# Performance work log

Measured on AMD Instinct MI355X. Metric: run time of the kernel, lower is better.

The kernel has to match this reference:

```python
import jax, jax.numpy as jnp
import numpy as np
import math

B, N, DMODEL, H = 8, 1024, 256, 8
HEAD_DIM = DMODEL // H


def setup_inputs() -> dict:
    key = jax.random.key(0)
    ks = jax.random.split(key, 8)
    x = jax.random.normal(ks[0], (B, N, DMODEL), dtype=jnp.float32)
    # symmetric-ish nonnegative pairwise distances
    adj = jax.random.uniform(ks[1], (B, N, N), dtype=jnp.float32) * 10.0
    mask = jax.random.uniform(ks[2], (B, N)) < 0.9  # bool, mostly valid nodes
    W_qkv = jax.random.normal(ks[3], (DMODEL, 3 * DMODEL), dtype=jnp.float32) / math.sqrt(DMODEL)
    b_qkv = jax.random.normal(ks[4], (3 * DMODEL,), dtype=jnp.float32) * 0.01
    shifts = jnp.arange(1.0, H + 1.0, dtype=jnp.float32)  # initial_shifts
    widths = jnp.ones((H,), dtype=jnp.float32)            # initial_widths
    # self_loop_W = 1/head_dim + U(0,1), non-trainable
    self_loop_w = 1.0 / HEAD_DIM + jax.random.uniform(ks[5], (H,), dtype=jnp.float32)
    return {"x": x, "adj": adj, "mask": mask, "W_qkv": W_qkv, "b_qkv": b_qkv,
            "shifts": shifts, "widths": widths, "self_loop_w": self_loop_w}


def reference(x, adj, mask, W_qkv, b_qkv, shifts, widths, self_loop_w):
    b, n, _ = x.shape
    h = shifts.shape[0]
    d = W_qkv.shape[1] // (3 * h)
    qkv = (x @ W_qkv + b_qkv).reshape(b, n, 3, h, d)
    qkv = jnp.transpose(qkv, (2, 0, 3, 1, 4))  # [3, B, H, N, D]
    Q, K, V = qkv[0], qkv[1], qkv[2]
    scores = jnp.einsum('bhnd,bhmd->bhnm', Q, K) / jnp.sqrt(jnp.float32(d))
    # Gaussian moire focus on adjacency distances, per head
    sh = shifts.reshape(1, h, 1, 1)
    w = jnp.maximum(widths, 0.5).reshape(1, h, 1, 1)
    moire = jnp.exp(-((adj[:, None, :, :] - sh) ** 2) / w)
    adjusted = scores + jnp.log(jnp.maximum(moire, 1e-6))
    eye = jnp.eye(n, dtype=adjusted.dtype)  # [N, N]
    adjusted = adjusted + eye * self_loop_w.reshape(1, h, 1, 1)
    mask2d = (mask[:, :, None] & mask[:, None, :])[:, None, :, :]  # [B,1,N,N]
    adjusted = jnp.where(mask2d, adjusted, jnp.float32(-1000000.0))
    attn = jax.nn.softmax(adjusted, axis=-1)
    out = jnp.einsum('bhnm,bhmd->bhnd', attn, V)
    return jnp.transpose(out, (0, 2, 1, 3)).reshape(b, n, h * d)
```

## Files before the change

kernel.cpp:

```cpp
#include <hip/hip_runtime.h>

#define BB 8
#define NN 1024
#define DM 256
#define HH 8
#define HD 32
#define TC 768

typedef __bf16 bf16x8 __attribute__((ext_vector_type(8)));
typedef float  f32x4  __attribute__((ext_vector_type(4)));

__global__ __launch_bounds__(256, 4) void qkv_gemm(
    const float* __restrict__ x, const float* __restrict__ W,
    const float* __restrict__ bias, __bf16* __restrict__ Qb,
    __bf16* __restrict__ Kb, __bf16* __restrict__ Vt)
{
  __shared__ __align__(16) __bf16 As[128][40];
  __shared__ __align__(16) __bf16 Bs[64][40];
  const int tid  = threadIdx.x;
  const int w    = tid >> 6, lane = tid & 63;
  const int n16  = lane & 15, quad = lane >> 4;
  const int m0   = blockIdx.y * 128, c0 = blockIdx.x * 64;

  const int arow = tid >> 1, ahalf = tid & 1;
  const int bc   = tid & 63, bkh = tid >> 6;

  f32x4 acc[2][4] = {};
  const f32x4 zero = {0.f, 0.f, 0.f, 0.f};
  (void)zero;

  for (int k0 = 0; k0 < DM; k0 += 32) {
    {
      const float* xa = &x[(size_t)(m0 + arow) * DM + k0 + ahalf * 16];
      float4 f0 = *(const float4*)&xa[0];
      float4 f1 = *(const float4*)&xa[4];
      float4 f2 = *(const float4*)&xa[8];
      float4 f3 = *(const float4*)&xa[12];
      bf16x8 a0, a1;
      a0[0]=(__bf16)f0.x; a0[1]=(__bf16)f0.y; a0[2]=(__bf16)f0.z; a0[3]=(__bf16)f0.w;
      a0[4]=(__bf16)f1.x; a0[5]=(__bf16)f1.y; a0[6]=(__bf16)f1.z; a0[7]=(__bf16)f1.w;
      a1[0]=(__bf16)f2.x; a1[1]=(__bf16)f2.y; a1[2]=(__bf16)f2.z; a1[3]=(__bf16)f2.w;
      a1[4]=(__bf16)f3.x; a1[5]=(__bf16)f3.y; a1[6]=(__bf16)f3.z; a1[7]=(__bf16)f3.w;
      *(bf16x8*)&As[arow][ahalf*16]     = a0;
      *(bf16x8*)&As[arow][ahalf*16 + 8] = a1;
    }
    {
      bf16x8 bv;
      #pragma unroll
      for (int j = 0; j < 8; ++j)
        bv[j] = (__bf16)W[(size_t)(k0 + bkh*8 + j) * TC + c0 + bc];
      *(bf16x8*)&Bs[bc][bkh*8] = bv;
    }
    __syncthreads();
    bf16x8 af0 = *(const bf16x8*)&As[w*32 + n16][quad*8];
    bf16x8 af1 = *(const bf16x8*)&As[w*32 + 16 + n16][quad*8];
    #pragma unroll
    for (int cb = 0; cb < 4; ++cb) {
      bf16x8 bf = *(const bf16x8*)&Bs[cb*16 + n16][quad*8];
      acc[0][cb] = __builtin_amdgcn_mfma_f32_16x16x32_bf16(af0, bf, acc[0][cb], 0, 0, 0);
      acc[1][cb] = __builtin_amdgcn_mfma_f32_16x16x32_bf16(af1, bf, acc[1][cb], 0, 0, 0);
    }
    __syncthreads();
  }

  #pragma unroll
  for (int cb = 0; cb < 4; ++cb) {
    const int c = c0 + cb*16 + n16;
    const float bv = bias[c];
    const int s = c >> 8, h = (c >> 5) & 7, dd = c & 31;
    #pragma unroll
    for (int mb = 0; mb < 2; ++mb) {
      #pragma unroll
      for (int r = 0; r < 4; ++r) {
        const int m = m0 + w*32 + mb*16 + quad*4 + r;
        const int bb = m >> 10, n = m & 1023;
        const __bf16 v = (__bf16)(acc[mb][cb][r] + bv);
        if (s == 2)
          Vt[((size_t)((bb*HH + h)*HD + dd))*NN + n] = v;
        else
          ((s == 0) ? Qb : Kb)[((size_t)((bb*HH + h)*NN + n))*HD + dd] = v;
      }
    }
  }
}

__global__ __launch_bounds__(256, 4) void attn_kernel(
    const __bf16* __restrict__ Q, const __bf16* __restrict__ K,
    const __bf16* __restrict__ Vt, const float* __restrict__ adj,
    const int* __restrict__ mask, const float* __restrict__ shifts,
    const float* __restrict__ widths, const float* __restrict__ slw,
    float* __restrict__ out)
{
  __shared__ __align__(16) __bf16 Qs[64][40];
  __shared__ __align__(16) __bf16 Ks[2][64][40];
  __shared__ __align__(16) __bf16 Vts[2][32][72];
  __shared__ __align__(16) __bf16 Ps[64][72];

  const int tid  = threadIdx.x;
  const int w    = tid >> 6, lane = tid & 63;
  const int n16  = lane & 15, quad = lane >> 4;
  const int bh   = blockIdx.x >> 4, qt = blockIdx.x & 15;
  const int b    = bh >> 3, h = bh & 7;
  const int q0   = qt * 64;

  const float L2E   = 1.4426950408889634f;
  const float sh    = shifts[h];
  const float ninvw = -L2E / fmaxf(widths[h], 0.5f);
  const float slv   = slw[h] * L2E;
  const float scl   = 0.17677669529663687f * L2E;
  const float LGEPS = -19.931568569324174f;
  const float MASKV = -28.0f;

  const int srow = tid >> 2, sseg = tid & 3;
  const int vd   = tid >> 3, vsg  = tid & 7;

  {
    const __bf16* Qg = Q + (size_t)(bh*NN + q0)*HD;
    *(bf16x8*)&Qs[srow][sseg*8] = *(const bf16x8*)&Qg[srow*HD + sseg*8];
  }
  const __bf16* Kg = K + (size_t)bh*NN*HD;
  const __bf16* Vg = Vt + (size_t)bh*HD*NN;
  {
    bf16x8 k0v = *(const bf16x8*)&Kg[srow*HD + sseg*8];
    bf16x8 v0v = *(const bf16x8*)&Vg[(size_t)vd*NN + vsg*8];
    *(bf16x8*)&Ks[0][srow][sseg*8] = k0v;
    *(bf16x8*)&Vts[0][vd][vsg*8]   = v0v;
  }
  int mq[4];
  #pragma unroll
  for (int r = 0; r < 4; ++r) mq[r] = mask[b*NN + q0 + w*16 + quad*4 + r];
  __syncthreads();

  const bf16x8 qf = *(const bf16x8*)&Qs[w*16 + n16][quad*8];
  const f32x4 zero = {0.f, 0.f, 0.f, 0.f};
  float l_r[4] = {0.f, 0.f, 0.f, 0.f};
  f32x4 o0 = zero, o1 = zero;

  const float* adjRow = adj + ((size_t)(b*NN + q0 + w*16 + quad*4))*NN;
  const int*   mrow   = mask + b*NN;

  #pragma unroll 2
  for (int jt = 0; jt < 16; ++jt) {
    const int cur = jt & 1;
    const int j0  = jt * 64;

    bf16x8 kn, vn;
    if (jt < 15) {
      kn = *(const bf16x8*)&Kg[(j0 + 64 + srow)*HD + sseg*8];
      vn = *(const bf16x8*)&Vg[(size_t)vd*NN + j0 + 64 + vsg*8];
    }

    int mj[4];
    #pragma unroll
    for (int cb = 0; cb < 4; ++cb) mj[cb] = mrow[j0 + cb*16 + n16];
    float av[4][4];
    #pragma unroll
    for (int r = 0; r < 4; ++r)
      #pragma unroll
      for (int cb = 0; cb < 4; ++cb)
        av[r][cb] = adjRow[(size_t)r*NN + j0 + cb*16 + n16];

    f32x4 s[4];
    #pragma unroll
    for (int cb = 0; cb < 4; ++cb) {
      bf16x8 kf = *(const bf16x8*)&Ks[cur][cb*16 + n16][quad*8];
      s[cb] = __builtin_amdgcn_mfma_f32_16x16x32_bf16(qf, kf, zero, 0, 0, 0);
    }

    #pragma unroll
    for (int r = 0; r < 4; ++r) {
      const int qg = q0 + w*16 + quad*4 + r;
      #pragma unroll
      for (int cb = 0; cb < 4; ++cb) {
        float d   = av[r][cb] - sh;
        float mo  = fmaxf(d*d*ninvw, LGEPS);
        float val = fmaf(s[cb][r], scl, mo);
        if (j0 + cb*16 + n16 == qg) val += slv;
        bool ok = (mq[r] != 0) && (mj[cb] != 0);
        val = ok ? val : MASKV;
        float p = exp2f(val);
        l_r[r] += p;
        Ps[w*16 + quad*4 + r][cb*16 + n16] = (__bf16)p;
      }
    }

    bf16x8 a0  = *(const bf16x8*)&Ps[w*16 + n16][quad*8];
    bf16x8 a1  = *(const bf16x8*)&Ps[w*16 + n16][32 + quad*8];
    bf16x8 b00 = *(const bf16x8*)&Vts[cur][n16][quad*8];
    bf16x8 b01 = *(const bf16x8*)&Vts[cur][n16][32 + quad*8];
    bf16x8 b10 = *(const bf16x8*)&Vts[cur][16 + n16][quad*8];
    bf16x8 b11 = *(const bf16x8*)&Vts[cur][16 + n16][32 + quad*8];
    o0 = __builtin_amdgcn_mfma_f32_16x16x32_bf16(a0, b00, o0, 0, 0, 0);
    o0 = __builtin_amdgcn_mfma_f32_16x16x32_bf16(a1, b01, o0, 0, 0, 0);
    o1 = __builtin_amdgcn_mfma_f32_16x16x32_bf16(a0, b10, o1, 0, 0, 0);
    o1 = __builtin_amdgcn_mfma_f32_16x16x32_bf16(a1, b11, o1, 0, 0, 0);

    if (jt < 15) {
      *(bf16x8*)&Ks[1 - cur][srow][sseg*8] = kn;
      *(bf16x8*)&Vts[1 - cur][vd][vsg*8]   = vn;
    }
    __syncthreads();
  }

  #pragma unroll
  for (int r = 0; r < 4; ++r) {
    float l = l_r[r];
    l += __shfl_xor(l, 1); l += __shfl_xor(l, 2);
    l += __shfl_xor(l, 4); l += __shfl_xor(l, 8);
    const float invl = 1.0f / l;
    const int n = q0 + w*16 + quad*4 + r;
    float* og = out + ((size_t)(b*NN + n))*DM + h*HD;
    og[n16]      = o0[r] * invl;
    og[16 + n16] = o1[r] * invl;
  }
}

extern "C" void kernel_launch(void* const* d_in, const int* in_sizes, int n_in,
                              void* d_out, int out_size, void* d_ws, size_t ws_size,
                              hipStream_t stream) {
  const float* x      = (const float*)d_in[0];
  const float* adj    = (const float*)d_in[1];
  const int*   mask   = (const int*)d_in[2];
  const float* W      = (const float*)d_in[3];
  const float* bias   = (const float*)d_in[4];
  const float* shifts = (const float*)d_in[5];
  const float* widths = (const float*)d_in[6];
  const float* slwp   = (const float*)d_in[7];
  float* out = (float*)d_out;

  __bf16* Qb = (__bf16*)d_ws;
  __bf16* Kb = Qb + (size_t)BB*HH*NN*HD;
  __bf16* Vt = Kb + (size_t)BB*HH*NN*HD;

  qkv_gemm<<<dim3(TC/64, (BB*NN)/128), 256, 0, stream>>>(x, W, bias, Qb, Kb, Vt);
  attn_kernel<<<dim3(BB*HH*(NN/64)), 256, 0, stream>>>(Qb, Kb, Vt, adj, mask,
                                                       shifts, widths, slwp, out);
}
```

Measured before the change: 163.5 us.

## Split attention over key halves with combine kernel, stage QKV epilogue through LDS

The attention kernel is templated to process half of the key range per block (grid y=2). It writes unnormalized partial outputs and row sums to workspace, and a new combine kernel adds the two halves and normalizes. This doubles block count to raise occupancy and parallelism, at the cost of an extra launch and additional fp32 traffic. The QKV GEMM epilogue now stages results through shared memory so Q/K/V^T stores are vectorized and coalesced. Other changes: Qs and Ps share LDS, the diagonal check is restricted to the diagonal tile, and exp2f is replaced with the hardware builtin.

Result: faster. 151.8 us (-7.2%).

```diff
diff --git a/kernel.cpp b/kernel.cpp
--- a/kernel.cpp
+++ b/kernel.cpp
@@ -8,6 +8,7 @@
 #define TC 768
 
 typedef __bf16 bf16x8 __attribute__((ext_vector_type(8)));
+typedef __bf16 bf16x4 __attribute__((ext_vector_type(4)));
 typedef float  f32x4  __attribute__((ext_vector_type(4)));
 
 __global__ __launch_bounds__(256, 4) void qkv_gemm(
@@ -15,19 +16,20 @@
     const float* __restrict__ bias, __bf16* __restrict__ Qb,
     __bf16* __restrict__ Kb, __bf16* __restrict__ Vt)
 {
-  __shared__ __align__(16) __bf16 As[128][40];
-  __shared__ __align__(16) __bf16 Bs[64][40];
+  __shared__ __align__(16) char U[18432];
+  __bf16* As = (__bf16*)U;
+  __bf16* Bs = (__bf16*)(U + 10240);
+
   const int tid  = threadIdx.x;
   const int w    = tid >> 6, lane = tid & 63;
   const int n16  = lane & 15, quad = lane >> 4;
   const int m0   = blockIdx.y * 128, c0 = blockIdx.x * 64;
+  const int bb   = m0 >> 10, n0 = m0 & 1023;
 
   const int arow = tid >> 1, ahalf = tid & 1;
   const int bc   = tid & 63, bkh = tid >> 6;
 
   f32x4 acc[2][4] = {};
-  const f32x4 zero = {0.f, 0.f, 0.f, 0.f};
-  (void)zero;
 
   for (int k0 = 0; k0 < DM; k0 += 32) {
     {
@@ -41,67 +43,99 @@
       a0[4]=(__bf16)f1.x; a0[5]=(__bf16)f1.y; a0[6]=(__bf16)f1.z; a0[7]=(__bf16)f1.w;
       a1[0]=(__bf16)f2.x; a1[1]=(__bf16)f2.y; a1[2]=(__bf16)f2.z; a1[3]=(__bf16)f2.w;
       a1[4]=(__bf16)f3.x; a1[5]=(__bf16)f3.y; a1[6]=(__bf16)f3.z; a1[7]=(__bf16)f3.w;
-      *(bf16x8*)&As[arow][ahalf*16]     = a0;
-      *(bf16x8*)&As[arow][ahalf*16 + 8] = a1;
+      *(bf16x8*)&As[arow*40 + ahalf*16]     = a0;
+      *(bf16x8*)&As[arow*40 + ahalf*16 + 8] = a1;
     }
     {
       bf16x8 bv;
       #pragma unroll
       for (int j = 0; j < 8; ++j)
         bv[j] = (__bf16)W[(size_t)(k0 + bkh*8 + j) * TC + c0 + bc];
-      *(bf16x8*)&Bs[bc][bkh*8] = bv;
-    }
-    __syncthreads();
-    bf16x8 af0 = *(const bf16x8*)&As[w*32 + n16][quad*8];
-    bf16x8 af1 = *(const bf16x8*)&As[w*32 + 16 + n16][quad*8];
+      *(bf16x8*)&Bs[bc*40 + bkh*8] = bv;
+    }
+    __syncthreads();
+    bf16x8 af0 = *(const bf16x8*)&As[(w*32 + n16)*40 + quad*8];
+    bf16x8 af1 = *(const bf16x8*)&As[(w*32 + 16 + n16)*40 + quad*8];
     #pragma unroll
     for (int cb = 0; cb < 4; ++cb) {
-      bf16x8 bf = *(const bf16x8*)&Bs[cb*16 + n16][quad*8];
+      bf16x8 bf = *(const bf16x8*)&Bs[(cb*16 + n16)*40 + quad*8];
       acc[0][cb] = __builtin_amdgcn_mfma_f32_16x16x32_bf16(af0, bf, acc[0][cb], 0, 0, 0);
       acc[1][cb] = __builtin_amdgcn_mfma_f32_16x16x32_bf16(af1, bf, acc[1][cb], 0, 0, 0);
     }
     __syncthreads();
   }
 
+  float bv[4];
   #pragma unroll
-  for (int cb = 0; cb < 4; ++cb) {
-    const int c = c0 + cb*16 + n16;
-    const float bv = bias[c];
-    const int s = c >> 8, h = (c >> 5) & 7, dd = c & 31;
-    #pragma unroll
-    for (int mb = 0; mb < 2; ++mb) {
-      #pragma unroll
-      for (int r = 0; r < 4; ++r) {
-        const int m = m0 + w*32 + mb*16 + quad*4 + r;
-        const int bb = m >> 10, n = m & 1023;
-        const __bf16 v = (__bf16)(acc[mb][cb][r] + bv);
-        if (s == 2)
-          Vt[((size_t)((bb*HH + h)*HD + dd))*NN + n] = v;
-        else
-          ((s == 0) ? Qb : Kb)[((size_t)((bb*HH + h)*NN + n))*HD + dd] = v;
+  for (int cb = 0; cb < 4; ++cb) bv[cb] = bias[c0 + cb*16 + n16];
+
+  if (c0 < 512) {
+    __bf16* Ct = (__bf16*)U;
+    #pragma unroll
+    for (int cb = 0; cb < 4; ++cb)
+      #pragma unroll
+      for (int mb = 0; mb < 2; ++mb)
+        #pragma unroll
+        for (int r = 0; r < 4; ++r)
+          Ct[(w*32 + mb*16 + quad*4 + r)*72 + cb*16 + n16] =
+              (__bf16)(acc[mb][cb][r] + bv[cb]);
+    __syncthreads();
+    const int chunk = tid & 3, hh = (tid >> 2) & 1, rbase = tid >> 3;
+    const int c_head = c0 + hh*32;
+    const int h = (c_head >> 5) & 7;
+    __bf16* base = (c_head >> 8) ? Kb : Qb;
+    #pragma unroll
+    for (int it = 0; it < 4; ++it) {
+      int rl = rbase + it*32;
+      bf16x8 v = *(const bf16x8*)&Ct[rl*72 + hh*32 + chunk*8];
+      *(bf16x8*)&base[((size_t)((bb*HH + h)*NN + n0 + rl))*HD + chunk*8] = v;
+    }
+  } else {
+    __bf16* CtT = (__bf16*)U;
+    #pragma unroll
+    for (int cb = 0; cb < 4; ++cb)
+      #pragma unroll
+      for (int mb = 0; mb < 2; ++mb) {
+        bf16x4 t;
+        #pragma unroll
+        for (int r = 0; r < 4; ++r) t[r] = (__bf16)(acc[mb][cb][r] + bv[cb]);
+        *(bf16x4*)&CtT[(cb*16 + n16)*136 + w*32 + mb*16 + quad*4] = t;
       }
-    }
+    __syncthreads();
+    const int col = tid >> 2, sg = tid & 3;
+    const int c = c0 + col;
+    const int h = (c >> 5) & 7, dd = c & 31;
+    __bf16* dst = &Vt[((size_t)((bb*HH + h)*HD + dd))*NN + n0 + sg*32];
+    const __bf16* srcp = &CtT[col*136 + sg*32];
+    #pragma unroll
+    for (int q2 = 0; q2 < 4; ++q2)
+      *(bf16x8*)&dst[q2*8] = *(const bf16x8*)&srcp[q2*8];
   }
 }
 
+template <int NJT, bool SPLIT>
 __global__ __launch_bounds__(256, 4) void attn_kernel(
     const __bf16* __restrict__ Q, const __bf16* __restrict__ K,
     const __bf16* __restrict__ Vt, const float* __restrict__ adj,
     const int* __restrict__ mask, const float* __restrict__ shifts,
     const float* __restrict__ widths, const float* __restrict__ slw,
-    float* __restrict__ out)
+    float* __restrict__ out, float* __restrict__ Opart,
+    float* __restrict__ lpart)
 {
-  __shared__ __align__(16) __bf16 Qs[64][40];
+  __shared__ __align__(16) char U[9216];
+  __bf16 (*Qs)[40] = (__bf16(*)[40])U;
+  __bf16 (*Ps)[72] = (__bf16(*)[72])U;
   __shared__ __align__(16) __bf16 Ks[2][64][40];
   __shared__ __align__(16) __bf16 Vts[2][32][72];
-  __shared__ __align__(16) __bf16 Ps[64][72];
 
   const int tid  = threadIdx.x;
   const int w    = tid >> 6, lane = tid & 63;
   const int n16  = lane & 15, quad = lane >> 4;
   const int bh   = blockIdx.x >> 4, qt = blockIdx.x & 15;
+  const int part = blockIdx.y;
   const int b    = bh >> 3, h = bh & 7;
   const int q0   = qt * 64;
+  const int jbase = part * NJT * 64;
 
   const float L2E   = 1.4426950408889634f;
   const float sh    = shifts[h];
@@ -121,17 +155,18 @@
   const __bf16* Kg = K + (size_t)bh*NN*HD;
   const __bf16* Vg = Vt + (size_t)bh*HD*NN;
   {
-    bf16x8 k0v = *(const bf16x8*)&Kg[srow*HD + sseg*8];
-    bf16x8 v0v = *(const bf16x8*)&Vg[(size_t)vd*NN + vsg*8];
-    *(bf16x8*)&Ks[0][srow][sseg*8] = k0v;
-    *(bf16x8*)&Vts[0][vd][vsg*8]   = v0v;
+    *(bf16x8*)&Ks[0][srow][sseg*8] =
+        *(const bf16x8*)&Kg[(jbase + srow)*HD + sseg*8];
+    *(bf16x8*)&Vts[0][vd][vsg*8] =
+        *(const bf16x8*)&Vg[(size_t)vd*NN + jbase + vsg*8];
   }
   int mq[4];
   #pragma unroll
   for (int r = 0; r < 4; ++r) mq[r] = mask[b*NN + q0 + w*16 + quad*4 + r];
   __syncthreads();
-
   const bf16x8 qf = *(const bf16x8*)&Qs[w*16 + n16][quad*8];
+  __syncthreads();
+
   const f32x4 zero = {0.f, 0.f, 0.f, 0.f};
   float l_r[4] = {0.f, 0.f, 0.f, 0.f};
   f32x4 o0 = zero, o1 = zero;
@@ -140,12 +175,12 @@
   const int*   mrow   = mask + b*NN;
 
   #pragma unroll 2
-  for (int jt = 0; jt < 16; ++jt) {
-    const int cur = jt & 1;
-    const int j0  = jt * 64;
+  for (int jtl = 0; jtl < NJT; ++jtl) {
+    const int cur = jtl & 1;
+    const int j0  = jbase + jtl * 64;
 
     bf16x8 kn, vn;
-    if (jt < 15) {
+    if (jtl < NJT - 1) {
       kn = *(const bf16x8*)&Kg[(j0 + 64 + srow)*HD + sseg*8];
       vn = *(const bf16x8*)&Vg[(size_t)vd*NN + j0 + 64 + vsg*8];
     }
@@ -167,20 +202,21 @@
       s[cb] = __builtin_amdgcn_mfma_f32_16x16x32_bf16(qf, kf, zero, 0, 0, 0);
     }
 
+    const bool diagtile = ((part * NJT + jtl) == qt);
     #pragma unroll
     for (int r = 0; r < 4; ++r) {
-      const int qg = q0 + w*16 + quad*4 + r;
+      const int rowl = w*16 + quad*4 + r;
       #pragma unroll
       for (int cb = 0; cb < 4; ++cb) {
         float d   = av[r][cb] - sh;
         float mo  = fmaxf(d*d*ninvw, LGEPS);
         float val = fmaf(s[cb][r], scl, mo);
-        if (j0 + cb*16 + n16 == qg) val += slv;
+        if (diagtile && (cb*16 + n16 == rowl)) val += slv;
         bool ok = (mq[r] != 0) && (mj[cb] != 0);
         val = ok ? val : MASKV;
-        float p = exp2f(val);
+        float p = __builtin_amdgcn_exp2f(val);
         l_r[r] += p;
-        Ps[w*16 + quad*4 + r][cb*16 + n16] = (__bf16)p;
+        Ps[rowl][cb*16 + n16] = (__bf16)p;
       }
     }
 
@@ -195,7 +231,7 @@
     o1 = __builtin_amdgcn_mfma_f32_16x16x32_bf16(a0, b10, o1, 0, 0, 0);
     o1 = __builtin_amdgcn_mfma_f32_16x16x32_bf16(a1, b11, o1, 0, 0, 0);
 
-    if (jt < 15) {
+    if (jtl < NJT - 1) {
       *(bf16x8*)&Ks[1 - cur][srow][sseg*8] = kn;
       *(bf16x8*)&Vts[1 - cur][vd][vsg*8]   = vn;
     }
@@ -207,12 +243,40 @@
     float l = l_r[r];
     l += __shfl_xor(l, 1); l += __shfl_xor(l, 2);
     l += __shfl_xor(l, 4); l += __shfl_xor(l, 8);
-    const float invl = 1.0f / l;
     const int n = q0 + w*16 + quad*4 + r;
-    float* og = out + ((size_t)(b*NN + n))*DM + h*HD;
-    og[n16]      = o0[r] * invl;
-    og[16 + n16] = o1[r] * invl;
-  }
+    if (SPLIT) {
+      float* og = Opart + ((size_t)(part*BB*HH + bh)*NN + n)*HD;
+      og[n16]      = o0[r];
+      og[16 + n16] = o1[r];
+      if (n16 == 0) lpart[(size_t)(part*BB*HH + bh)*NN + n] = l;
+    } else {
+      const float invl = 1.0f / l;
+      float* og = out + ((size_t)(b*NN + n))*DM + h*HD;
+      og[n16]      = o0[r] * invl;
+      og[16 + n16] = o1[r] * invl;
+    }
+  }
+}
+
+__global__ __launch_bounds__(256) void combine_kernel(
+    const float* __restrict__ Opart, const float* __restrict__ lpart,
+    float* __restrict__ out)
+{
+  const size_t e = (size_t)blockIdx.x * 256 + threadIdx.x;
+  const int c = (int)((e << 2) & 255);
+  const int n = (int)((e >> 6) & 1023);
+  const int b = (int)(e >> 16);
+  const int h = c >> 5, d = c & 31;
+  const size_t row = (size_t)(b*HH + h)*NN + n;
+  const size_t i0  = row*HD + d;
+  const size_t ps  = (size_t)BB*HH*NN*HD;
+  const float4 a0 = *(const float4*)&Opart[i0];
+  const float4 a1 = *(const float4*)&Opart[ps + i0];
+  const float  l  = lpart[row] + lpart[(size_t)BB*HH*NN + row];
+  const float invl = 1.0f / l;
+  float4 o = {(a0.x + a1.x)*invl, (a0.y + a1.y)*invl,
+              (a0.z + a1.z)*invl, (a0.w + a1.w)*invl};
+  *(float4*)&out[((size_t)(b*NN + n))*DM + c] = o;
 }
 
 extern "C" void kernel_launch(void* const* d_in, const int* in_sizes, int n_in,
@@ -228,11 +292,22 @@
   const float* slwp   = (const float*)d_in[7];
   float* out = (float*)d_out;
 
+  const size_t BHND = (size_t)BB*HH*NN*HD;
   __bf16* Qb = (__bf16*)d_ws;
-  __bf16* Kb = Qb + (size_t)BB*HH*NN*HD;
-  __bf16* Vt = Kb + (size_t)BB*HH*NN*HD;
+  __bf16* Kb = Qb + BHND;
+  __bf16* Vt = Kb + BHND;
+  float*  Opart = (float*)((char*)d_ws + 3*BHND*sizeof(__bf16));
+  float*  lpart = Opart + 2*BHND;
+  const size_t need = 3*BHND*2 + 2*BHND*4 + 2*(size_t)BB*HH*NN*4;
 
   qkv_gemm<<<dim3(TC/64, (BB*NN)/128), 256, 0, stream>>>(x, W, bias, Qb, Kb, Vt);
-  attn_kernel<<<dim3(BB*HH*(NN/64)), 256, 0, stream>>>(Qb, Kb, Vt, adj, mask,
-                                                       shifts, widths, slwp, out);
+
+  if (ws_size >= need) {
+    attn_kernel<8, true><<<dim3(BB*HH*(NN/64), 2), 256, 0, stream>>>(
+        Qb, Kb, Vt, adj, mask, shifts, widths, slwp, out, Opart, lpart);
+    combine_kernel<<<(int)(BHND/4/256), 256, 0, stream>>>(Opart, lpart, out);
+  } else {
+    attn_kernel<16, false><<<dim3(BB*HH*(NN/64), 1), 256, 0, stream>>>(
+        Qb, Kb, Vt, adj, mask, shifts, widths, slwp, out, Opart, lpart);
+  }
 }
```
